# Performance work log

Hardware: AMD Instinct MI355X
Metric: run time of the kernel (lower is better)

## Reference

```python
import jax, jax.numpy as jnp
import numpy as np

S = 4  # MC samples


def _gat_layer(x, mask, w, a_src, a_dst, bias):
    # x: (b,n,fin)  w: (H,fin,fout)  mask: (b,n,n) bool
    h = jnp.einsum('bnf,hfo->bhno', x, w)                      # (b,H,n,fout)
    th = jnp.tanh(h)
    att_src = jnp.einsum('bhno,ho->bhn', th, a_src)
    att_dst = jnp.einsum('bhno,ho->bhn', th, a_dst)
    logits = jax.nn.leaky_relu(att_src[:, :, :, None] + att_dst[:, :, None, :], 0.2)
    logits = jnp.where(mask[:, None, :, :], logits, jnp.float32(-1e9))
    att = jax.nn.softmax(logits, axis=-1)                      # (b,H,n,n)
    out = jnp.einsum('bhij,bhjo->bhio', att, h) + bias         # (b,H,n,fout)
    return out, att


def setup_inputs() -> dict:
    key = jax.random.key(0)
    ks = jax.random.split(key, 11)
    b, n, f0, emb_d = 128, 128, 64, 64
    H1, f1, H2, f2 = 8, 16, 1, 2
    fin1 = f0 + emb_d            # 128 (n_units[0] += 64)
    fin2 = H1 * f1               # 128 (heads concatenated between layers)
    x = jax.random.normal(ks[0], (b, n, f0), jnp.float32)
    emb = jax.random.normal(ks[1], (b, n, emb_d), jnp.float32)
    adj = jax.random.randint(ks[2], (b, n, n), 0, 2).astype(jnp.int32)
    adj = jnp.maximum(adj, jnp.eye(n, dtype=jnp.int32)[None])  # self-loops keep softmax rows valid
    w1 = jax.random.normal(ks[3], (S, H1, fin1, f1), jnp.float32) * 0.1
    a_src1 = jax.random.normal(ks[4], (S, H1, f1), jnp.float32) * 0.1
    a_dst1 = jax.random.normal(ks[5], (S, H1, f1), jnp.float32) * 0.1
    b1 = jax.random.normal(ks[6], (f1,), jnp.float32) * 0.1
    w2 = jax.random.normal(ks[7], (S, H2, fin2, f2), jnp.float32) * 0.1
    a_src2 = jax.random.normal(ks[8], (S, H2, f2), jnp.float32) * 0.1
    a_dst2 = jax.random.normal(ks[9], (S, H2, f2), jnp.float32) * 0.1
    b2 = jax.random.normal(ks[10], (f2,), jnp.float32) * 0.1
    return dict(x=x, emb=emb, adj=adj, w1=w1, a_src1=a_src1, a_dst1=a_dst1, b1=b1,
                w2=w2, a_src2=a_src2, a_dst2=a_dst2, b2=b2)


def reference(x, emb, adj, w1, a_src1, a_dst1, b1, w2, a_src2, a_dst2, b2):
    mask = adj.astype(bool)
    x0 = jnp.concatenate([x, emb], axis=-1)                    # (b,n,128)
    b, n = x0.shape[0], x0.shape[1]
    xs = jnp.broadcast_to(x0, (S,) + x0.shape)                 # same input for each MC sample
    layer = jax.vmap(_gat_layer, in_axes=(0, None, 0, 0, 0, None))
    # layer 1 (per-sample variational weights), ELU activation
    h1, att1 = layer(xs, mask, w1, a_src1, a_dst1, b1)         # h1: (S,b,H1,n,f1)
    h1 = jax.nn.elu(h1)
    # concat heads: transpose(1,2).view(bs,n,-1)
    xs2 = jnp.transpose(h1, (0, 1, 3, 2, 4)).reshape(S, b, n, -1)
    # layer 2 (last layer): no activation, mean over heads
    h2, att2 = layer(xs2, mask, w2, a_src2, a_dst2, b2)        # (S,b,1,n,2)
    out = h2.mean(axis=2)                                      # (S,b,n,2)
    logp = jax.nn.log_softmax(out, axis=-1)[:, :, -1, :]       # (S,b,2) -> ego node
    result = jnp.mean(logp, axis=0)                            # var_mean -> mean (return_uncertainty=False)
    return result
```

## Files before the change

kernel.cpp:

```cpp
#include <hip/hip_runtime.h>
#include <stdint.h>
#include <math.h>

typedef __attribute__((ext_vector_type(8))) short short8;
typedef __attribute__((ext_vector_type(4))) float floatx4;

#define L_HF    0
#define L_SRC   16384
#define L_DST   18432
#define L_MASK  20480
#define L_H2P   22528
#define L_SIZE  26624

union F8 { short8 s8; uint32_t u[4]; };

#if __has_builtin(__builtin_amdgcn_exp2f)
#define EXP2F __builtin_amdgcn_exp2f
#else
#define EXP2F exp2f
#endif
#define LOG2E 1.4426950408889634f

__device__ __forceinline__ uint32_t packbf(float a, float b){
  uint32_t ua = __float_as_uint(a), ub = __float_as_uint(b);
  uint32_t ra = (ua + 0x7fffu + ((ua>>16)&1u)) >> 16;
  uint32_t rb = (ub + 0x7fffu + ((ub>>16)&1u)) >> 16;
  return ra | (rb<<16);
}
__device__ __forceinline__ uint32_t packbf_t(float a, float b){
  return __builtin_amdgcn_perm(__float_as_uint(b), __float_as_uint(a), 0x07060302u);
}
__device__ __forceinline__ float fast_tanh(float x){
  float e = __expf(2.f*x);
  return 1.f - 2.f*__builtin_amdgcn_rcpf(e + 1.f);
}
__device__ __forceinline__ float mexp2(float l, uint32_t mb, int jj){
  float e = EXP2F(l);
  int sm = ((int)(mb << (31-jj))) >> 31;
  return __int_as_float(__float_as_int(e) & sm);
}
__device__ __forceinline__ float red16(float x){
  x += __int_as_float(__builtin_amdgcn_update_dpp(0, __float_as_int(x), 0x128, 0xf, 0xf, true));
  x += __int_as_float(__builtin_amdgcn_update_dpp(0, __float_as_int(x), 0x124, 0xf, 0xf, true));
  x += __int_as_float(__builtin_amdgcn_update_dpp(0, __float_as_int(x), 0x122, 0xf, 0xf, true));
  x += __int_as_float(__builtin_amdgcn_update_dpp(0, __float_as_int(x), 0x121, 0xf, 0xf, true));
  return x;
}

__global__ __launch_bounds__(512,6) void gat_fused(
    const float* __restrict__ x,  const float* __restrict__ emb,
    const int* __restrict__ adj,  const float* __restrict__ w1,
    const float* __restrict__ a_src1, const float* __restrict__ a_dst1,
    const float* __restrict__ b1, const float* __restrict__ w2,
    float* __restrict__ ws_h2)
{
  __shared__ __align__(16) char smem[L_SIZE];
  char*     hf    = smem + L_HF;
  uint32_t* hf_u  = (uint32_t*)(smem + L_HF);
  float*    src_l = (float*)(smem + L_SRC);
  float*    dst_l = (float*)(smem + L_DST);
  uint32_t* mask_l= (uint32_t*)(smem + L_MASK);
  const uint4* mask4 = (const uint4*)(smem + L_MASK);
  float2*   h2p   = (float2*)(smem + L_H2P);

  const int t    = threadIdx.x;
  const int blk  = blockIdx.x;
  const int s    = blk >> 8;
  const int bb   = (blk & 255) >> 1;
  const int half = blk & 1;
  const int lane = t & 63, w = t >> 6;
  const int of = lane & 15, kg = lane >> 4;

  const int arow = w*16 + of;
  const float* xrow = x   + ((size_t)bb*128 + arow)*64;
  const float* erow = emb + ((size_t)bb*128 + arow)*64;
  short8 af[4];
  #pragma unroll
  for (int ks=0; ks<4; ++ks){
    int k = ks*32 + kg*8;
    const float* p = (k<64) ? (xrow+k) : (erow + (k-64));
    float4 f0 = *(const float4*)p, f1 = *(const float4*)(p+4);
    F8 fr;
    fr.u[0]=packbf(f0.x,f0.y); fr.u[1]=packbf(f0.z,f0.w);
    fr.u[2]=packbf(f1.x,f1.y); fr.u[3]=packbf(f1.z,f1.w);
    af[ks]=fr.s8;
  }

  {
    const float* w1s = w1 + (size_t)s*16384 + half*8192;
    #pragma unroll
    for (int r=0; r<2; ++r){
      int q = t + r*512;
      int ql = q & 63, ks = (q>>6)&3, ct = q>>8;
      const float* wp = w1s + ct*2048 + (ks*32 + (ql>>4)*8)*16 + (ql&15);
      F8 fr;
      fr.u[0]=packbf(wp[0],  wp[16]);
      fr.u[1]=packbf(wp[32], wp[48]);
      fr.u[2]=packbf(wp[64], wp[80]);
      fr.u[3]=packbf(wp[96], wp[112]);
      *(short8*)(hf + ((ct*4+ks)*64 + ql)*16) = fr.s8;
    }
  }

  {
    const int* adjb = adj + (size_t)bb*16384;
    #pragma unroll 4
    for (int rr=0; rr<16; ++rr){
      const int row = w*16 + rr;
      const int* ar = adjb + row*128;
      uint64_t m0 = __ballot(ar[lane] != 0);
      uint64_t m1 = __ballot(ar[64+lane] != 0);
      if (lane == 0)
        ((uint4*)mask_l)[row] = make_uint4((uint32_t)m0,(uint32_t)(m0>>32),
                                           (uint32_t)m1,(uint32_t)(m1>>32));
    }
  }
  __syncthreads();

  floatx4 acc[4];
  #pragma unroll
  for (int ct=0; ct<4; ++ct) acc[ct]=(floatx4){0.f,0.f,0.f,0.f};
  #pragma unroll
  for (int ct=0; ct<4; ++ct)
    #pragma unroll
    for (int ks=0; ks<4; ++ks){
      short8 bfr = *(const short8*)(hf + ((ct*4+ks)*64 + lane)*16);
      acc[ct] = __builtin_amdgcn_mfma_f32_16x16x32_bf16(af[ks], bfr, acc[ct], 0,0,0);
    }
  __syncthreads();

  const int ks_h = w>>1, kgp = (w&1)*2 + (kg>>1), vv = (kg&1)*2;
  #pragma unroll
  for (int ct=0; ct<4; ++ct){
    const int ghd = half*4 + ct;
    float asv = a_src1[s*128 + ghd*16 + of] * LOG2E;
    float adv = a_dst1[s*128 + ghd*16 + of] * LOG2E;
    float ps[4], pd[4];
    #pragma unroll
    for (int r=0; r<4; ++r){
      float th = fast_tanh(acc[ct][r]);
      ps[r] = red16(th*asv); pd[r] = red16(th*adv);
    }
    if (of==0){
      #pragma unroll
      for (int r=0; r<4; ++r){
        int i = w*16 + kg*4 + r;
        src_l[ct*128+i]=ps[r]; dst_l[ct*128+i]=pd[r];
      }
    }
    uint32_t p0 = packbf(acc[ct][0], acc[ct][1]);
    uint32_t p1 = packbf(acc[ct][2], acc[ct][3]);
    uint32_t* dsth = hf_u + ((ct*4+ks_h)*64 + kgp*16 + of)*4 + vv;
    *(uint2*)dsth = make_uint2(p0, p1);
  }
  __syncthreads();

  const int lhd = w >> 1;
  const int ghd = half*4 + lhd;
  const int rtb = (w&1)*4;
  float b1v  = b1[of];
  float w2c0 = w2[s*256 + (ghd*16+of)*2 + 0];
  float w2c1 = w2[s*256 + (ghd*16+of)*2 + 1];
  F8 onesf;
  onesf.u[0]=0x3F803F80u; onesf.u[1]=0x3F803F80u;
  onesf.u[2]=0x3F803F80u; onesf.u[3]=0x3F803F80u;

  #pragma unroll
  for (int pp=0; pp<2; ++pp){
    const int rt0 = rtb + pp*2, rt1 = rt0 + 1;
    const int im0 = rt0*16 + of, im1 = rt1*16 + of;
    float srcv0 = src_l[lhd*128 + im0];
    float srcv1 = src_l[lhd*128 + im1];
    uint4 mrow0 = mask4[im0];
    uint4 mrow1 = mask4[im1];
    floatx4 acc20 = (floatx4){0.f,0.f,0.f,0.f};
    floatx4 acc21 = (floatx4){0.f,0.f,0.f,0.f};
    floatx4 accz0 = (floatx4){0.f,0.f,0.f,0.f};
    floatx4 accz1 = (floatx4){0.f,0.f,0.f,0.f};
    #pragma unroll
    for (int ks=0; ks<4; ++ks){
      const float* dp = dst_l + lhd*128 + ks*32 + kg*8;
      float4 d0 = *(const float4*)dp, d1 = *(const float4*)(dp+4);
      short8 hbk = *(const short8*)(hf + ((lhd*4+ks)*64 + lane)*16);
      uint32_t mw0 = (ks==0)?mrow0.x:(ks==1)?mrow0.y:(ks==2)?mrow0.z:mrow0.w;
      uint32_t mw1 = (ks==0)?mrow1.x:(ks==1)?mrow1.y:(ks==2)?mrow1.z:mrow1.w;
      uint32_t mb0 = mw0 >> (kg*8);
      uint32_t mb1 = mw1 >> (kg*8);
      float dj[8] = {d0.x,d0.y,d0.z,d0.w,d1.x,d1.y,d1.z,d1.w};
      F8 fr0, fr1;
      #pragma unroll
      for (int jp=0; jp<4; ++jp){
        const int j0 = 2*jp, j1 = 2*jp+1;
        float ta0 = srcv0 + dj[j0], ta1 = srcv0 + dj[j1];
        float tb0 = srcv1 + dj[j0], tb1 = srcv1 + dj[j1];
        float la0 = fmaxf(ta0, 0.2f*ta0), la1 = fmaxf(ta1, 0.2f*ta1);
        float lb0 = fmaxf(tb0, 0.2f*tb0), lb1 = fmaxf(tb1, 0.2f*tb1);
        float ea0 = mexp2(la0, mb0, j0), ea1 = mexp2(la1, mb0, j1);
        float eb0 = mexp2(lb0, mb1, j0), eb1 = mexp2(lb1, mb1, j1);
        fr0.u[jp] = packbf_t(ea0, ea1);
        fr1.u[jp] = packbf_t(eb0, eb1);
      }
      acc20 = __builtin_amdgcn_mfma_f32_16x16x32_bf16(fr0.s8, hbk,      acc20, 0,0,0);
      accz0 = __builtin_amdgcn_mfma_f32_16x16x32_bf16(fr0.s8, onesf.s8, accz0, 0,0,0);
      acc21 = __builtin_amdgcn_mfma_f32_16x16x32_bf16(fr1.s8, hbk,      acc21, 0,0,0);
      accz1 = __builtin_amdgcn_mfma_f32_16x16x32_bf16(fr1.s8, onesf.s8, accz1, 0,0,0);
    }
    #pragma unroll
    for (int pr=0; pr<2; ++pr){
      const int rt = pr ? rt1 : rt0;
      floatx4 a2 = pr ? acc21 : acc20;
      floatx4 az = pr ? accz1 : accz0;
      float pc0[4], pc1[4];
      #pragma unroll
      for (int r=0; r<4; ++r){
        float zi = __builtin_amdgcn_rcpf(az[r]);
        float o  = fmaf(a2[r], zi, b1v);
        float oe = (o>0.f) ? o : (__expf(o)-1.f);
        pc0[r] = red16(oe*w2c0);
        pc1[r] = red16(oe*w2c1);
      }
      if (of==0){
        #pragma unroll
        for (int r=0; r<4; ++r){
          int i = rt*16 + kg*4 + r;
          h2p[lhd*128 + i] = make_float2(pc0[r], pc1[r]);
        }
      }
    }
  }
  __syncthreads();

  if (t < 256){
    const int jn = t>>1, cc = t&1;
    float hv = 0.f;
    #pragma unroll
    for (int hd2=0; hd2<4; ++hd2){
      float2 p = h2p[hd2*128+jn];
      hv += cc ? p.y : p.x;
    }
    ws_h2[(size_t)blk*256 + t] = hv;
  }
}

__global__ __launch_bounds__(256) void gat_tail(
    const float* __restrict__ ws_h2, const int* __restrict__ adj,
    const float* __restrict__ a_src2, const float* __restrict__ a_dst2,
    const float* __restrict__ b2, float* __restrict__ out)
{
  __shared__ float d2_l[128];
  __shared__ float red[16];
  __shared__ float srcE;
  const int bb = blockIdx.x, t = threadIdx.x;
  const int jn = t>>1, cc = t&1, lane = t&63, w = t>>6;
  const uint32_t bit = (adj[((size_t)bb*128+127)*128 + jn] != 0) ? 1u : 0u;
  float acc0=0.f, acc1=0.f;
  for (int s=0; s<4; ++s){
    float hv = ws_h2[(size_t)(s*256 + bb*2 + 0)*256 + t]
             + ws_h2[(size_t)(s*256 + bb*2 + 1)*256 + t];
    float th2 = fast_tanh(hv);
    float ps2 = th2*a_src2[s*2+cc];
    float pd2 = th2*a_dst2[s*2+cc];
    ps2 += __shfl_xor(ps2,1);
    pd2 += __shfl_xor(pd2,1);
    if (s) __syncthreads();
    if (cc==0) d2_l[jn]=pd2;
    if (t==254) srcE=ps2;
    __syncthreads();
    float t0 = srcE + d2_l[jn];
    float lg = fmaxf(t0, 0.2f*t0);
    float v  = bit ? lg : -1e9f;
    float mloc = v;
    #pragma unroll
    for (int off=32; off>=1; off>>=1) mloc = fmaxf(mloc, __shfl_xor(mloc,off));
    if (lane==0) red[w]=mloc;
    __syncthreads();
    float M = fmaxf(fmaxf(red[0],red[1]), fmaxf(red[2],red[3]));
    float e2 = __expf(v-M);
    float vA = e2*hv;
    float vZ = (cc==0) ? e2 : 0.f;
    #pragma unroll
    for (int off=2; off<=32; off<<=1){ vA+=__shfl_xor(vA,off); vZ+=__shfl_xor(vZ,off); }
    if (lane==0){ red[4+w]=vA; red[12+w]=vZ; }
    if (lane==1){ red[8+w]=vA; }
    __syncthreads();
    if (t==0){
      float S0 = red[4]+red[5]+red[6]+red[7];
      float S1 = red[8]+red[9]+red[10]+red[11];
      float Z  = red[12]+red[13]+red[14]+red[15];
      float o0 = S0/Z + b2[0];
      float o1 = S1/Z + b2[1];
      float mm = fmaxf(o0,o1);
      float lse = mm + logf(__expf(o0-mm)+__expf(o1-mm));
      acc0 += 0.25f*(o0 - lse);
      acc1 += 0.25f*(o1 - lse);
    }
  }
  if (t==0){ out[bb*2+0]=acc0; out[bb*2+1]=acc1; }
}

extern "C" void kernel_launch(void* const* d_in, const int* in_sizes, int n_in,
                              void* d_out, int out_size, void* d_ws, size_t ws_size,
                              hipStream_t stream) {
  const float* x      = (const float*)d_in[0];
  const float* emb    = (const float*)d_in[1];
  const int*   adj    = (const int*)d_in[2];
  const float* w1     = (const float*)d_in[3];
  const float* a_src1 = (const float*)d_in[4];
  const float* a_dst1 = (const float*)d_in[5];
  const float* b1     = (const float*)d_in[6];
  const float* w2     = (const float*)d_in[7];
  const float* a_src2 = (const float*)d_in[8];
  const float* a_dst2 = (const float*)d_in[9];
  const float* b2     = (const float*)d_in[10];

  float* ws_h2 = (float*)d_ws;

  gat_fused<<<dim3(1024), dim3(512), 0, stream>>>(x, emb, adj, w1, a_src1, a_dst1,
                                                  b1, w2, ws_h2);
  gat_tail<<<dim3(128), dim3(256), 0, stream>>>(ws_h2, adj, a_src2, a_dst2, b2,
                                                (float*)d_out);
}
```

Baseline: 124.6 us.

## Precompute adjacency bitmask in separate kernel and truncate bf16 packing

Moves the adjacency-to-bitmask ballot conversion out of the fused kernel into a new pre-pass kernel that writes a packed mask to workspace. Previously each of the 8 blocks per batch (4 samples × 2 halves) re-read the full 64KB int adjacency. Now each reads a 2KB mask. It also switches bf16 packing from round-to-nearest to truncation via perm, and computes tanh with exp2 and fma. This adds a kernel launch and slightly changes numerics through truncation.

```diff
diff --git a/kernel.cpp b/kernel.cpp
--- a/kernel.cpp
+++ b/kernel.cpp
@@ -12,6 +12,8 @@
 #define L_H2P   22528
 #define L_SIZE  26624
 
+#define WS_H2_BYTES   (1024*256*4)
+
 union F8 { short8 s8; uint32_t u[4]; };
 
 #if __has_builtin(__builtin_amdgcn_exp2f)
@@ -19,7 +21,8 @@
 #else
 #define EXP2F exp2f
 #endif
-#define LOG2E 1.4426950408889634f
+#define LOG2E  1.4426950408889634f
+#define LOG2E2 2.8853900817779268f
 
 __device__ __forceinline__ uint32_t packbf(float a, float b){
   uint32_t ua = __float_as_uint(a), ub = __float_as_uint(b);
@@ -31,8 +34,8 @@
   return __builtin_amdgcn_perm(__float_as_uint(b), __float_as_uint(a), 0x07060302u);
 }
 __device__ __forceinline__ float fast_tanh(float x){
-  float e = __expf(2.f*x);
-  return 1.f - 2.f*__builtin_amdgcn_rcpf(e + 1.f);
+  float e = EXP2F(LOG2E2*x);
+  return fmaf(-2.f, __builtin_amdgcn_rcpf(e + 1.f), 1.f);
 }
 __device__ __forceinline__ float mexp2(float l, uint32_t mb, int jj){
   float e = EXP2F(l);
@@ -47,12 +50,25 @@
   return x;
 }
 
+__global__ void mask_build(const int* __restrict__ adj, uint32_t* __restrict__ mask_ws) {
+  const int t = threadIdx.x;
+  const int row = blockIdx.x*4 + (t>>6);
+  const int lane = t & 63;
+  const int* ar = adj + (size_t)row*128;
+  uint64_t m0 = __ballot(ar[lane] != 0);
+  uint64_t m1 = __ballot(ar[64+lane] != 0);
+  if (lane == 0) {
+    ((uint4*)mask_ws)[row] = make_uint4((uint32_t)m0, (uint32_t)(m0>>32),
+                                        (uint32_t)m1, (uint32_t)(m1>>32));
+  }
+}
+
 __global__ __launch_bounds__(512,6) void gat_fused(
     const float* __restrict__ x,  const float* __restrict__ emb,
-    const int* __restrict__ adj,  const float* __restrict__ w1,
+    const float* __restrict__ w1,
     const float* __restrict__ a_src1, const float* __restrict__ a_dst1,
     const float* __restrict__ b1, const float* __restrict__ w2,
-    float* __restrict__ ws_h2)
+    const uint32_t* __restrict__ mask_ws, float* __restrict__ ws_h2)
 {
   __shared__ __align__(16) char smem[L_SIZE];
   char*     hf    = smem + L_HF;
@@ -71,6 +87,8 @@
   const int lane = t & 63, w = t >> 6;
   const int of = lane & 15, kg = lane >> 4;
 
+  mask_l[t] = mask_ws[(size_t)bb*512 + t];
+
   const int arow = w*16 + of;
   const float* xrow = x   + ((size_t)bb*128 + arow)*64;
   const float* erow = emb + ((size_t)bb*128 + arow)*64;
@@ -81,8 +99,8 @@
     const float* p = (k<64) ? (xrow+k) : (erow + (k-64));
     float4 f0 = *(const float4*)p, f1 = *(const float4*)(p+4);
     F8 fr;
-    fr.u[0]=packbf(f0.x,f0.y); fr.u[1]=packbf(f0.z,f0.w);
-    fr.u[2]=packbf(f1.x,f1.y); fr.u[3]=packbf(f1.z,f1.w);
+    fr.u[0]=packbf_t(f0.x,f0.y); fr.u[1]=packbf_t(f0.z,f0.w);
+    fr.u[2]=packbf_t(f1.x,f1.y); fr.u[3]=packbf_t(f1.z,f1.w);
     af[ks]=fr.s8;
   }
 
@@ -94,25 +112,11 @@
       int ql = q & 63, ks = (q>>6)&3, ct = q>>8;
       const float* wp = w1s + ct*2048 + (ks*32 + (ql>>4)*8)*16 + (ql&15);
       F8 fr;
-      fr.u[0]=packbf(wp[0],  wp[16]);
-      fr.u[1]=packbf(wp[32], wp[48]);
-      fr.u[2]=packbf(wp[64], wp[80]);
-      fr.u[3]=packbf(wp[96], wp[112]);
+      fr.u[0]=packbf_t(wp[0],  wp[16]);
+      fr.u[1]=packbf_t(wp[32], wp[48]);
+      fr.u[2]=packbf_t(wp[64], wp[80]);
+      fr.u[3]=packbf_t(wp[96], wp[112]);
       *(short8*)(hf + ((ct*4+ks)*64 + ql)*16) = fr.s8;
-    }
-  }
-
-  {
-    const int* adjb = adj + (size_t)bb*16384;
-    #pragma unroll 4
-    for (int rr=0; rr<16; ++rr){
-      const int row = w*16 + rr;
-      const int* ar = adjb + row*128;
-      uint64_t m0 = __ballot(ar[lane] != 0);
-      uint64_t m1 = __ballot(ar[64+lane] != 0);
-      if (lane == 0)
-        ((uint4*)mask_l)[row] = make_uint4((uint32_t)m0,(uint32_t)(m0>>32),
-                                           (uint32_t)m1,(uint32_t)(m1>>32));
     }
   }
   __syncthreads();
@@ -313,10 +317,12 @@
   const float* a_dst2 = (const float*)d_in[9];
   const float* b2     = (const float*)d_in[10];
 
-  float* ws_h2 = (float*)d_ws;
-
-  gat_fused<<<dim3(1024), dim3(512), 0, stream>>>(x, emb, adj, w1, a_src1, a_dst1,
-                                                  b1, w2, ws_h2);
+  float*    ws_h2   = (float*)d_ws;
+  uint32_t* mask_ws = (uint32_t*)((char*)d_ws + WS_H2_BYTES);
+
+  mask_build<<<dim3(4096), dim3(256), 0, stream>>>(adj, mask_ws);
+  gat_fused<<<dim3(1024), dim3(512), 0, stream>>>(x, emb, w1, a_src1, a_dst1,
+                                                  b1, w2, mask_ws, ws_h2);
   gat_tail<<<dim3(128), dim3(256), 0, stream>>>(ws_h2, adj, a_src2, a_dst2, b2,
                                                 (float*)d_out);
 }
```

Measured after the change: 122.6 us. About the same (-1.6%).
